# Kernel optimization log

Hardware: AMD Instinct MI355X
Metric: run time of the kernel (lower is better)

Reference implementation:

```python
import jax, jax.numpy as jnp
import numpy as np

EPS = 1e-12

def _l2(v):
    return v / (jnp.linalg.norm(v) + EPS)

def _sn_weight(w, u):
    # Spectral normalization, one power iteration with stored u (not updated here).
    cout = w.shape[-1]
    wm = w.reshape(-1, cout)              # [d, cout]
    u = jax.lax.stop_gradient(u)
    v = _l2(wm @ u)                       # [d]
    u2 = _l2(wm.T @ v)                    # [cout]
    sigma = v @ (wm @ u2)
    return w / sigma

def _conv1x1(x, w, u):
    # 1x1 conv, no bias, with spectral-normalized kernel. x: [B,H,W,Cin], w: [1,1,Cin,Cout]
    wbar = _sn_weight(w, u)[0, 0]         # [Cin, Cout]
    return jnp.einsum('bhwc,co->bhwo', x, wbar)

def _maxpool2(x):
    # 2x2 max pool, stride 2, valid. x: [B,H,W,C]
    B, H, W, C = x.shape
    return x.reshape(B, H // 2, 2, W // 2, 2, C).max(axis=(2, 4))

def setup_inputs() -> dict:
    key = jax.random.key(0)
    ks = jax.random.split(key, 9)
    B, H, W, C = 16, 64, 64, 64
    inp = {
        'x': jax.random.normal(ks[0], (B, H, W, C), jnp.float32),
        'w_theta': jax.random.normal(ks[1], (1, 1, C, C // 8), jnp.float32) * 0.05,
        'u_theta': jax.random.normal(ks[2], (C // 8,), jnp.float32),
        'w_phi': jax.random.normal(ks[3], (1, 1, C, C // 8), jnp.float32) * 0.05,
        'u_phi': jax.random.normal(ks[4], (C // 8,), jnp.float32),
        'w_g': jax.random.normal(ks[5], (1, 1, C, C // 2), jnp.float32) * 0.05,
        'u_g': jax.random.normal(ks[6], (C // 2,), jnp.float32),
        'w_o': jax.random.normal(ks[7], (1, 1, C // 2, C), jnp.float32) * 0.05,
        'u_o': jax.random.normal(ks[8], (C,), jnp.float32),
        'gamma': jnp.zeros((1,), jnp.float32),
    }
    return inp

def reference(x, w_theta, u_theta, w_phi, u_phi, w_g, u_g, w_o, u_o, gamma):
    B, H, W, C = x.shape
    theta = _conv1x1(x, w_theta, u_theta).reshape(B, H * W, C // 8)          # [B,HW,C/8]
    phi = _maxpool2(_conv1x1(x, w_phi, u_phi)).reshape(B, H * W // 4, C // 8)  # [B,HW/4,C/8]
    attn = jax.nn.softmax(jnp.einsum('bnk,bmk->bnm', theta, phi), axis=-1)   # [B,HW,HW/4]
    g = _maxpool2(_conv1x1(x, w_g, u_g)).reshape(B, H * W // 4, C // 2)      # [B,HW/4,C/2]
    attn_g = jnp.einsum('bnm,bmc->bnc', attn, g).reshape(B, H, W, C // 2)    # [B,H,W,C/2]
    attn_g = _conv1x1(attn_g, w_o, u_o)                                      # [B,H,W,C]
    return x + gamma * attn_g
```

## Files before the change

kernel.cpp:

```cpp
#include <hip/hip_runtime.h>
#include <hip/hip_bf16.h>
#include <math.h>

#define NB 16
#define NPIX 4096
#define MPOOL 1024

typedef __attribute__((ext_vector_type(8))) short bf16x8;
typedef __attribute__((ext_vector_type(4))) float f32x4;

__device__ inline unsigned short f2bf(float f) {
    __hip_bfloat16 h = __float2bfloat16(f);
    return *reinterpret_cast<unsigned short*>(&h);
}

#if defined(__has_builtin)
#if __has_builtin(__builtin_amdgcn_cvt_pk_bf16_f32)
#define HAVE_PK_BF16 1
#endif
#endif
__device__ inline unsigned pack_bf16(float a, float b) {
#ifdef HAVE_PK_BF16
    typedef __bf16 bf16v2 __attribute__((ext_vector_type(2)));
    bf16v2 v = __builtin_amdgcn_cvt_pk_bf16_f32(a, b);
    unsigned u;
    __builtin_memcpy(&u, &v, 4);
    return u;
#else
    unsigned ua = __float_as_uint(a) + 0x8000u;
    unsigned ub = __float_as_uint(b) + 0x8000u;
    return __builtin_amdgcn_perm(ua, ub, 0x03020706u);
#endif
}


__device__ inline float wave_sum64(float v) {
    #pragma unroll
    for (int off = 32; off >= 1; off >>= 1) v += __shfl_xor(v, off);
    return v;
}

__global__ void sn_kernel(const float* __restrict__ w_theta, const float* __restrict__ u_theta,
                          const float* __restrict__ w_phi,   const float* __restrict__ u_phi,
                          const float* __restrict__ w_g,     const float* __restrict__ u_g,
                          const float* __restrict__ w_o,     const float* __restrict__ u_o,
                          unsigned short* __restrict__ wcT_bf,
                          unsigned short* __restrict__ woT_bf) {
    const float* w; const float* u; unsigned short* dst; int d, cout;
    switch (blockIdx.x) {
      case 0:  w = w_theta; u = u_theta; dst = wcT_bf;           d = 64; cout = 8;  break;
      case 1:  w = w_phi;   u = u_phi;   dst = wcT_bf + 8 * 64;  d = 64; cout = 8;  break;
      case 2:  w = w_g;     u = u_g;     dst = wcT_bf + 16 * 64; d = 64; cout = 32; break;
      default: w = w_o;     u = u_o;     dst = woT_bf;           d = 32; cout = 64; break;
    }
    __shared__ float sv[64];
    __shared__ float su2[64];
    const int tid = threadIdx.x;

    float vi = 0.f;
    if (tid < d) for (int j = 0; j < cout; ++j) vi += w[tid * cout + j] * u[j];
    float nn = wave_sum64(vi * vi);
    vi *= 1.0f / (sqrtf(nn) + 1e-12f);
    sv[tid] = vi;
    __syncthreads();

    float u2j = 0.f;
    if (tid < cout) for (int i = 0; i < d; ++i) u2j += w[i * cout + tid] * sv[i];
    float nn2 = wave_sum64(u2j * u2j);
    u2j *= 1.0f / (sqrtf(nn2) + 1e-12f);
    su2[tid] = u2j;
    __syncthreads();

    float ti = 0.f;
    if (tid < d) for (int j = 0; j < cout; ++j) ti += w[tid * cout + j] * su2[j];
    float sig = wave_sum64(vi * ti);
    const float inv_sig = 1.0f / sig;
    for (int idx = tid; idx < d * cout; idx += 64) {
        const int i = idx / cout, j = idx - i * cout;
        dst[j * d + i] = f2bf(w[idx] * inv_sig);
    }
}

__global__ __launch_bounds__(256) void conv_all_kernel(const float* __restrict__ x,
                                                       const unsigned short* __restrict__ wcT_bf,
                                                       unsigned short* __restrict__ theta_bf,
                                                       unsigned short* __restrict__ phi_bf,
                                                       unsigned short* __restrict__ gT_bf) {
    __shared__ unsigned short sx[128 * 72];
    __shared__ unsigned short sw[48 * 72];

    const int tid = threadIdx.x;
    const int b  = blockIdx.x >> 5;
    const int hp = blockIdx.x & 31;
    const int h0 = hp * 2;

    const float4* xb4 = (const float4*)(x + (((size_t)b * NPIX) + h0 * 64) * 64);
    #pragma unroll
    for (int it = 0; it < 8; ++it) {
        const int li = tid + it * 256;
        float4 v = xb4[li];
        const int px = li >> 4, c4 = li & 15;
        uint2 pk;
        pk.x = pack_bf16(v.x, v.y);
        pk.y = pack_bf16(v.z, v.w);
        *(uint2*)(&sx[px * 72 + c4 * 4]) = pk;
    }
    for (int idx = tid; idx < 48 * 64; idx += 256) {
        const int col = idx >> 6, k = idx & 63;
        sw[col * 72 + k] = wcT_bf[idx];
    }
    __syncthreads();

    const int w    = tid >> 6;
    const int lane = tid & 63;
    const int quad = lane >> 4;
    const int lcol = lane & 15;
    const int w0   = w * 16;

    bf16x8 a[2][2];
    #pragma unroll
    for (int hh = 0; hh < 2; ++hh)
        #pragma unroll
        for (int kc = 0; kc < 2; ++kc)
            a[hh][kc] = *(const bf16x8*)(sx + (hh * 64 + w0 + lcol) * 72 + kc * 32 + quad * 8);

    f32x4 acc[2][3];
    #pragma unroll
    for (int ct = 0; ct < 3; ++ct) {
        bf16x8 b0 = *(const bf16x8*)(sw + (ct * 16 + lcol) * 72 + 0 * 32 + quad * 8);
        bf16x8 b1 = *(const bf16x8*)(sw + (ct * 16 + lcol) * 72 + 1 * 32 + quad * 8);
        #pragma unroll
        for (int hh = 0; hh < 2; ++hh) {
            f32x4 c = __builtin_amdgcn_mfma_f32_16x16x32_bf16(a[hh][0], b0, (f32x4)0.0f, 0, 0, 0);
            acc[hh][ct] = __builtin_amdgcn_mfma_f32_16x16x32_bf16(a[hh][1], b1, c, 0, 0, 0);
        }
    }

    if (lcol < 8) {
        #pragma unroll
        for (int hh = 0; hh < 2; ++hh) {
            const size_t rowbase = (size_t)b * NPIX + (h0 + hh) * 64 + w0 + quad * 4;
            #pragma unroll
            for (int r = 0; r < 4; ++r)
                theta_bf[(rowbase + r) * 8 + lcol] = f2bf(acc[hh][0][r]);
        }
    }
    const int mcb = hp * 32 + (w0 >> 1) + quad * 2;
    if (lcol >= 8) {
        #pragma unroll
        for (int r2 = 0; r2 < 2; ++r2) {
            float pe = fmaxf(fmaxf(acc[0][0][2 * r2], acc[0][0][2 * r2 + 1]),
                             fmaxf(acc[1][0][2 * r2], acc[1][0][2 * r2 + 1]));
            phi_bf[((size_t)b * MPOOL + mcb + r2) * 8 + (lcol - 8)] = f2bf(pe);
        }
    }
    #pragma unroll
    for (int ct = 1; ct < 3; ++ct) {
        const int cg = (ct - 1) * 16 + lcol;
        #pragma unroll
        for (int r2 = 0; r2 < 2; ++r2) {
            float pe = fmaxf(fmaxf(acc[0][ct][2 * r2], acc[0][ct][2 * r2 + 1]),
                             fmaxf(acc[1][ct][2 * r2], acc[1][ct][2 * r2 + 1]));
            gT_bf[((size_t)b * 32 + cg) * MPOOL + mcb + r2] = f2bf(pe);
        }
    }
}

__global__ __launch_bounds__(512) void attn_kernel(const unsigned short* __restrict__ theta_bf,
                                                   const unsigned short* __restrict__ phi_bf,
                                                   const unsigned short* __restrict__ gT_bf,
                                                   const unsigned short* __restrict__ woT_bf,
                                                   const float* __restrict__ x,
                                                   const float* __restrict__ gamma,
                                                   float* __restrict__ out) {
    __shared__ unsigned short sphi[MPOOL * 8];
    __shared__ unsigned short sg[2][32 * 264];
    __shared__ unsigned short sP[8][16 * 72];
    __shared__ unsigned short swo[64 * 40];

    const int tid  = threadIdx.x;
    const int b    = blockIdx.x >> 5;
    const int qb   = blockIdx.x & 31;
    const int w    = tid >> 6;
    const int lane = tid & 63;
    const int quad = lane >> 4;
    const int lcol = lane & 15;

    {
        const float4* src = (const float4*)(phi_bf + (size_t)b * (MPOOL * 8));
        float4* dst = (float4*)sphi;
        dst[2 * tid]     = src[2 * tid];
        dst[2 * tid + 1] = src[2 * tid + 1];
    }
    for (int idx = tid; idx < 64 * 32; idx += 512) {
        const int n = idx >> 5, k = idx & 31;
        swo[n * 40 + k] = woT_bf[idx];
    }
    const unsigned short* gTb = gT_bf + (size_t)b * (32 * MPOOL);
    const int prow = tid >> 4, pseg = tid & 15;
    {
        const float4* src = (const float4*)(gTb + prow * MPOOL + pseg * 16);
        float4 r0 = src[0], r1 = src[1];
        float4* dst = (float4*)(&sg[0][prow * 264 + pseg * 16]);
        dst[0] = r0; dst[1] = r1;
    }
    const int q0w = qb * 128 + w * 16;
    bf16x8 tfrag = (bf16x8)(short)0;
    if (quad == 0)
        tfrag = *(const bf16x8*)(theta_bf + ((size_t)b * NPIX + q0w + lcol) * 8);
    __syncthreads();

    f32x4 olo = (f32x4)0.0f, ohi = (f32x4)0.0f;
    float ls = 0.f;
    unsigned short* sPw = sP[w];

    float4 pre0, pre1;
    for (int t = 0; t < 4; ++t) {
        if (t < 3) {
            const float4* src = (const float4*)(gTb + prow * MPOOL + (t + 1) * 256 + pseg * 16);
            pre0 = src[0]; pre1 = src[1];
        }
        const unsigned short* sgb = sg[t & 1];
        for (int cb = 0; cb < 4; ++cb) {
            const int m0 = t * 256 + cb * 64;
            f32x4 s[4];
            #pragma unroll
            for (int sc = 0; sc < 4; ++sc) {
                bf16x8 pf = *(const bf16x8*)(sphi + (size_t)(m0 + sc * 16 + lcol) * 8);
                s[sc] = __builtin_amdgcn_mfma_f32_16x16x32_bf16(pf, tfrag, (f32x4)0.0f, 0, 0, 0);
            }
            #pragma unroll
            for (int sc = 0; sc < 4; ++sc) {
                float e0 = __expf(s[sc][0]);
                float e1 = __expf(s[sc][1]);
                float e2 = __expf(s[sc][2]);
                float e3 = __expf(s[sc][3]);
                ls += (e0 + e1) + (e2 + e3);
                uint2 pk2;
                pk2.x = (unsigned)f2bf(e0) | ((unsigned)f2bf(e1) << 16);
                pk2.y = (unsigned)f2bf(e2) | ((unsigned)f2bf(e3) << 16);
                *(uint2*)(sPw + lcol * 72 + sc * 16 + quad * 4) = pk2;
            }
            asm volatile("s_waitcnt lgkmcnt(0)" ::: "memory");
            #pragma unroll
            for (int pkk = 0; pkk < 2; ++pkk) {
                bf16x8 afrag = *(const bf16x8*)(sPw + lcol * 72 + pkk * 32 + quad * 8);
                bf16x8 bg0 = *(const bf16x8*)(sgb + lcol * 264 + cb * 64 + pkk * 32 + quad * 8);
                olo = __builtin_amdgcn_mfma_f32_16x16x32_bf16(afrag, bg0, olo, 0, 0, 0);
                bf16x8 bg1 = *(const bf16x8*)(sgb + (16 + lcol) * 264 + cb * 64 + pkk * 32 + quad * 8);
                ohi = __builtin_amdgcn_mfma_f32_16x16x32_bf16(afrag, bg1, ohi, 0, 0, 0);
            }
        }
        if (t < 3) {
            float4* dst = (float4*)(&sg[(t + 1) & 1][prow * 264 + pseg * 16]);
            dst[0] = pre0; dst[1] = pre1;
        }
        __syncthreads();
    }

    ls += __shfl_xor(ls, 16);
    ls += __shfl_xor(ls, 32);
    const float invq = 1.0f / ls;

    #pragma unroll
    for (int r = 0; r < 4; ++r) {
        sPw[(quad * 4 + r) * 40 + lcol]      = f2bf(olo[r]);
        sPw[(quad * 4 + r) * 40 + 16 + lcol] = f2bf(ohi[r]);
    }
    asm volatile("s_waitcnt lgkmcnt(0)" ::: "memory");
    bf16x8 agf = *(const bf16x8*)(sPw + lcol * 40 + quad * 8);

    const float gmi = gamma[0] * invq;
    const size_t pixbase = ((size_t)b * NPIX + q0w + lcol) * 64;
    #pragma unroll
    for (int ct = 0; ct < 4; ++ct) {
        bf16x8 wa = *(const bf16x8*)(swo + (ct * 16 + lcol) * 40 + quad * 8);
        f32x4 oc = __builtin_amdgcn_mfma_f32_16x16x32_bf16(wa, agf, (f32x4)0.0f, 0, 0, 0);
        const float4 xv = *(const float4*)(x + pixbase + ct * 16 + quad * 4);
        float4 ov;
        ov.x = xv.x + gmi * oc[0];
        ov.y = xv.y + gmi * oc[1];
        ov.z = xv.z + gmi * oc[2];
        ov.w = xv.w + gmi * oc[3];
        *(float4*)(out + pixbase + ct * 16 + quad * 4) = ov;
    }
}

extern "C" void kernel_launch(void* const* d_in, const int* in_sizes, int n_in,
                              void* d_out, int out_size, void* d_ws, size_t ws_size,
                              hipStream_t stream) {
    const float* x       = (const float*)d_in[0];
    const float* w_theta = (const float*)d_in[1];
    const float* u_theta = (const float*)d_in[2];
    const float* w_phi   = (const float*)d_in[3];
    const float* u_phi   = (const float*)d_in[4];
    const float* w_g     = (const float*)d_in[5];
    const float* u_g     = (const float*)d_in[6];
    const float* w_o     = (const float*)d_in[7];
    const float* u_o     = (const float*)d_in[8];
    const float* gamma   = (const float*)d_in[9];
    float* out = (float*)d_out;

    unsigned short* u16base  = (unsigned short*)d_ws;
    unsigned short* wcT_bf   = u16base;
    unsigned short* woT_bf   = u16base + 3072;
    unsigned short* theta_bf = u16base + 5120;
    unsigned short* phi_bf   = u16base + 529408;
    unsigned short* gT_bf    = u16base + 660480;

    sn_kernel<<<4, 64, 0, stream>>>(w_theta, u_theta, w_phi, u_phi, w_g, u_g, w_o, u_o,
                                    wcT_bf, woT_bf);
    conv_all_kernel<<<512, 256, 0, stream>>>(x, wcT_bf, theta_bf, phi_bf, gT_bf);
    attn_kernel<<<512, 512, 0, stream>>>(theta_bf, phi_bf, gT_bf, woT_bf, x, gamma, out);
}
```

Before: 122.8 us.

## Fuse spectral norm into conv and attention kernels, stage conv outputs in LDS

Removes the separate spectral-norm launch. Each conv block now computes the three inverse sigmas with one wave per weight, using shuffles instead of shared memory, and scales the weights as it loads them. Each attention block does the same for w_o. The conv epilogue writes theta, phi and pooled g into LDS first, then stores them to global memory as coalesced float4 writes instead of scattered 2-byte stores. The cost is redundant sigma computation in every block plus extra barriers.

```diff
diff --git a/kernel.cpp b/kernel.cpp
--- a/kernel.cpp
+++ b/kernel.cpp
@@ -40,59 +40,56 @@
     return v;
 }
 
-__global__ void sn_kernel(const float* __restrict__ w_theta, const float* __restrict__ u_theta,
-                          const float* __restrict__ w_phi,   const float* __restrict__ u_phi,
-                          const float* __restrict__ w_g,     const float* __restrict__ u_g,
-                          const float* __restrict__ w_o,     const float* __restrict__ u_o,
-                          unsigned short* __restrict__ wcT_bf,
-                          unsigned short* __restrict__ woT_bf) {
-    const float* w; const float* u; unsigned short* dst; int d, cout;
-    switch (blockIdx.x) {
-      case 0:  w = w_theta; u = u_theta; dst = wcT_bf;           d = 64; cout = 8;  break;
-      case 1:  w = w_phi;   u = u_phi;   dst = wcT_bf + 8 * 64;  d = 64; cout = 8;  break;
-      case 2:  w = w_g;     u = u_g;     dst = wcT_bf + 16 * 64; d = 64; cout = 32; break;
-      default: w = w_o;     u = u_o;     dst = woT_bf;           d = 32; cout = 64; break;
-    }
-    __shared__ float sv[64];
-    __shared__ float su2[64];
-    const int tid = threadIdx.x;
-
+template<int D, int COUT>
+__device__ float sn_inv_sigma(const float* __restrict__ w, const float* __restrict__ u) {
+    const int lane = threadIdx.x & 63;
     float vi = 0.f;
-    if (tid < d) for (int j = 0; j < cout; ++j) vi += w[tid * cout + j] * u[j];
+    if (lane < D) {
+        #pragma unroll 8
+        for (int j = 0; j < COUT; ++j) vi += w[lane * COUT + j] * u[j];
+    }
     float nn = wave_sum64(vi * vi);
     vi *= 1.0f / (sqrtf(nn) + 1e-12f);
-    sv[tid] = vi;
-    __syncthreads();
-
-    float u2j = 0.f;
-    if (tid < cout) for (int i = 0; i < d; ++i) u2j += w[i * cout + tid] * sv[i];
-    float nn2 = wave_sum64(u2j * u2j);
-    u2j *= 1.0f / (sqrtf(nn2) + 1e-12f);
-    su2[tid] = u2j;
-    __syncthreads();
+
+    float u2 = 0.f;
+    #pragma unroll 8
+    for (int i = 0; i < D; ++i) {
+        float vv = __shfl(vi, i);
+        if (lane < COUT) u2 += w[i * COUT + lane] * vv;
+    }
+    float nn2 = wave_sum64(u2 * u2);
+    u2 *= 1.0f / (sqrtf(nn2) + 1e-12f);
 
     float ti = 0.f;
-    if (tid < d) for (int j = 0; j < cout; ++j) ti += w[tid * cout + j] * su2[j];
+    #pragma unroll 8
+    for (int j = 0; j < COUT; ++j) {
+        float uv = __shfl(u2, j);
+        if (lane < D) ti += w[lane * COUT + j] * uv;
+    }
     float sig = wave_sum64(vi * ti);
-    const float inv_sig = 1.0f / sig;
-    for (int idx = tid; idx < d * cout; idx += 64) {
-        const int i = idx / cout, j = idx - i * cout;
-        dst[j * d + i] = f2bf(w[idx] * inv_sig);
-    }
+    return 1.0f / sig;
 }
 
 __global__ __launch_bounds__(256) void conv_all_kernel(const float* __restrict__ x,
-                                                       const unsigned short* __restrict__ wcT_bf,
+                                                       const float* __restrict__ w_theta, const float* __restrict__ u_theta,
+                                                       const float* __restrict__ w_phi,   const float* __restrict__ u_phi,
+                                                       const float* __restrict__ w_g,     const float* __restrict__ u_g,
                                                        unsigned short* __restrict__ theta_bf,
                                                        unsigned short* __restrict__ phi_bf,
                                                        unsigned short* __restrict__ gT_bf) {
     __shared__ unsigned short sx[128 * 72];
     __shared__ unsigned short sw[48 * 72];
-
-    const int tid = threadIdx.x;
-    const int b  = blockIdx.x >> 5;
-    const int hp = blockIdx.x & 31;
-    const int h0 = hp * 2;
+    __shared__ float s_inv[3];
+
+    const int tid  = threadIdx.x;
+    const int b    = blockIdx.x >> 5;
+    const int hp   = blockIdx.x & 31;
+    const int h0   = hp * 2;
+    const int wv   = tid >> 6;
+    const int lane = tid & 63;
+    const int quad = lane >> 4;
+    const int lcol = lane & 15;
+    const int w0   = wv * 16;
 
     const float4* xb4 = (const float4*)(x + (((size_t)b * NPIX) + h0 * 64) * 64);
     #pragma unroll
@@ -105,17 +102,25 @@
         pk.y = pack_bf16(v.z, v.w);
         *(uint2*)(&sx[px * 72 + c4 * 4]) = pk;
     }
-    for (int idx = tid; idx < 48 * 64; idx += 256) {
-        const int col = idx >> 6, k = idx & 63;
-        sw[col * 72 + k] = wcT_bf[idx];
-    }
-    __syncthreads();
-
-    const int w    = tid >> 6;
-    const int lane = tid & 63;
-    const int quad = lane >> 4;
-    const int lcol = lane & 15;
-    const int w0   = w * 16;
+    if (wv == 0)      { float iv = sn_inv_sigma<64, 8>(w_theta, u_theta); if (lane == 0) s_inv[0] = iv; }
+    else if (wv == 1) { float iv = sn_inv_sigma<64, 8>(w_phi,   u_phi);   if (lane == 0) s_inv[1] = iv; }
+    else if (wv == 2) { float iv = sn_inv_sigma<64, 32>(w_g,    u_g);     if (lane == 0) s_inv[2] = iv; }
+    __syncthreads();
+
+    {
+        const float i0 = s_inv[0], i1 = s_inv[1], i2 = s_inv[2];
+        #pragma unroll
+        for (int it = 0; it < 12; ++it) {
+            const int idx = tid + it * 256;
+            const int col = idx >> 6, k = idx & 63;
+            float wvf, inv;
+            if (col < 8)       { wvf = w_theta[k * 8 + col];        inv = i0; }
+            else if (col < 16) { wvf = w_phi[k * 8 + (col - 8)];    inv = i1; }
+            else               { wvf = w_g[k * 32 + (col - 16)];    inv = i2; }
+            sw[col * 72 + k] = f2bf(wvf * inv);
+        }
+    }
+    __syncthreads();
 
     bf16x8 a[2][2];
     #pragma unroll
@@ -135,23 +140,26 @@
             acc[hh][ct] = __builtin_amdgcn_mfma_f32_16x16x32_bf16(a[hh][1], b1, c, 0, 0, 0);
         }
     }
-
+    __syncthreads();
+
+    unsigned short* th = sx;
+    unsigned short* ph = sx + 1024;
+    unsigned short* gg = sx + 1280;
+    const int ml = (w0 >> 1) + quad * 2;
     if (lcol < 8) {
         #pragma unroll
         for (int hh = 0; hh < 2; ++hh) {
-            const size_t rowbase = (size_t)b * NPIX + (h0 + hh) * 64 + w0 + quad * 4;
+            const int pix = hh * 64 + w0 + quad * 4;
             #pragma unroll
             for (int r = 0; r < 4; ++r)
-                theta_bf[(rowbase + r) * 8 + lcol] = f2bf(acc[hh][0][r]);
-        }
-    }
-    const int mcb = hp * 32 + (w0 >> 1) + quad * 2;
-    if (lcol >= 8) {
+                th[(pix + r) * 8 + lcol] = f2bf(acc[hh][0][r]);
+        }
+    } else {
         #pragma unroll
         for (int r2 = 0; r2 < 2; ++r2) {
             float pe = fmaxf(fmaxf(acc[0][0][2 * r2], acc[0][0][2 * r2 + 1]),
                              fmaxf(acc[1][0][2 * r2], acc[1][0][2 * r2 + 1]));
-            phi_bf[((size_t)b * MPOOL + mcb + r2) * 8 + (lcol - 8)] = f2bf(pe);
+            ph[(ml + r2) * 8 + (lcol - 8)] = f2bf(pe);
         }
     }
     #pragma unroll
@@ -161,7 +169,24 @@
         for (int r2 = 0; r2 < 2; ++r2) {
             float pe = fmaxf(fmaxf(acc[0][ct][2 * r2], acc[0][ct][2 * r2 + 1]),
                              fmaxf(acc[1][ct][2 * r2], acc[1][ct][2 * r2 + 1]));
-            gT_bf[((size_t)b * 32 + cg) * MPOOL + mcb + r2] = f2bf(pe);
+            gg[cg * 32 + ml + r2] = f2bf(pe);
+        }
+    }
+    __syncthreads();
+
+    const float4* sv4 = (const float4*)sx;
+    float4* th4 = (float4*)(theta_bf + ((size_t)b * NPIX + hp * 128) * 8);
+    float4* ph4 = (float4*)(phi_bf + ((size_t)b * MPOOL + hp * 32) * 8);
+    for (int idx = tid; idx < 288; idx += 256) {
+        float4 v = sv4[idx];
+        if (idx < 128) {
+            th4[idx] = v;
+        } else if (idx < 160) {
+            ph4[idx - 128] = v;
+        } else {
+            const int gi = idx - 160;
+            const int ch = gi >> 2, part = gi & 3;
+            *(float4*)(gT_bf + ((size_t)b * 32 + ch) * MPOOL + hp * 32 + part * 8) = v;
         }
     }
 }
@@ -169,7 +194,8 @@
 __global__ __launch_bounds__(512) void attn_kernel(const unsigned short* __restrict__ theta_bf,
                                                    const unsigned short* __restrict__ phi_bf,
                                                    const unsigned short* __restrict__ gT_bf,
-                                                   const unsigned short* __restrict__ woT_bf,
+                                                   const float* __restrict__ w_o,
+                                                   const float* __restrict__ u_o,
                                                    const float* __restrict__ x,
                                                    const float* __restrict__ gamma,
                                                    float* __restrict__ out) {
@@ -192,10 +218,6 @@
         dst[2 * tid]     = src[2 * tid];
         dst[2 * tid + 1] = src[2 * tid + 1];
     }
-    for (int idx = tid; idx < 64 * 32; idx += 512) {
-        const int n = idx >> 5, k = idx & 31;
-        swo[n * 40 + k] = woT_bf[idx];
-    }
     const unsigned short* gTb = gT_bf + (size_t)b * (32 * MPOOL);
     const int prow = tid >> 4, pseg = tid & 15;
     {
@@ -208,7 +230,13 @@
     bf16x8 tfrag = (bf16x8)(short)0;
     if (quad == 0)
         tfrag = *(const bf16x8*)(theta_bf + ((size_t)b * NPIX + q0w + lcol) * 8);
-    __syncthreads();
+    const float wo_inv = sn_inv_sigma<32, 64>(w_o, u_o);
+    __syncthreads();
+
+    for (int idx = tid; idx < 64 * 32; idx += 512) {
+        const int n = idx >> 5, k = idx & 31;
+        swo[n * 40 + k] = f2bf(w_o[k * 64 + n] * wo_inv);
+    }
 
     f32x4 olo = (f32x4)0.0f, ohi = (f32x4)0.0f;
     float ls = 0.f;
@@ -302,14 +330,11 @@
     float* out = (float*)d_out;
 
     unsigned short* u16base  = (unsigned short*)d_ws;
-    unsigned short* wcT_bf   = u16base;
-    unsigned short* woT_bf   = u16base + 3072;
-    unsigned short* theta_bf = u16base + 5120;
-    unsigned short* phi_bf   = u16base + 529408;
-    unsigned short* gT_bf    = u16base + 660480;
-
-    sn_kernel<<<4, 64, 0, stream>>>(w_theta, u_theta, w_phi, u_phi, w_g, u_g, w_o, u_o,
-                                    wcT_bf, woT_bf);
-    conv_all_kernel<<<512, 256, 0, stream>>>(x, wcT_bf, theta_bf, phi_bf, gT_bf);
-    attn_kernel<<<512, 512, 0, stream>>>(theta_bf, phi_bf, gT_bf, woT_bf, x, gamma, out);
-}
+    unsigned short* theta_bf = u16base;
+    unsigned short* phi_bf   = u16base + 524288;
+    unsigned short* gT_bf    = u16base + 655360;
+
+    conv_all_kernel<<<512, 256, 0, stream>>>(x, w_theta, u_theta, w_phi, u_phi, w_g, u_g,
+                                             theta_bf, phi_bf, gT_bf);
+    attn_kernel<<<512, 512, 0, stream>>>(theta_bf, phi_bf, gT_bf, w_o, u_o, x, gamma, out);
+}
```

After: 135.8 us. 10.6% more time.
